# Kernel optimization log

Hardware: AMD Instinct MI355X
Metric: run time of the kernel (lower is better)

The kernel has to match this reference:

```python
import jax, jax.numpy as jnp
import numpy as np

N_ENTITIES = 100000
N_RELATIONS = 1000
D = 100   # embedding_size
K = 4     # tensor slices
B = 4096  # batch


def setup_inputs() -> dict:
    key = jax.random.key(0)
    k1, k2, k3, k4, k5, k6, k7, k8 = jax.random.split(key, 8)
    return {
        "heads": jax.random.randint(k1, (B,), 0, N_ENTITIES),
        "tails": jax.random.randint(k2, (B,), 0, N_ENTITIES),
        "relations": jax.random.randint(k3, (B,), 0, N_RELATIONS),
        # parameters, matching tf.random_uniform(0, 1)
        "entity_embedding": jax.random.uniform(k4, (N_ENTITIES, D), dtype=jnp.float32),
        "W": jax.random.uniform(k5, (N_RELATIONS, K, D, D), dtype=jnp.float32),
        "V": jax.random.uniform(k6, (N_RELATIONS, K, 2 * D), dtype=jnp.float32),
        "Bp": jax.random.uniform(k7, (N_RELATIONS, K), dtype=jnpp_f32 if False else jnp.float32),
        "U": jax.random.uniform(k8, (N_RELATIONS, K), dtype=jnp.float32),
    }


def reference(heads, tails, relations, entity_embedding, W, V, Bp, U):
    # gathers
    e1 = entity_embedding[heads]          # [B, D]
    e2 = entity_embedding[tails]          # [B, D]
    w = W[relations]                      # [B, K, D, D]
    v = V[relations]                      # [B, K, 2D]
    b = Bp[relations]                     # [B, K]
    u = U[relations]                      # [B, K]

    # g_a = v @ [e1; e2]
    e12 = jnp.concatenate([e1, e2], axis=1)           # [B, 2D]
    g_a = jnp.einsum('bkm,bm->bk', v, e12)            # [B, K]
    # g_b = e1^T W_k e2 (bilinear tensor product)
    g_b = jnp.einsum('bd,bkde,be->bk', e1, w, e2)     # [B, K]

    score = jnp.einsum('bk,bk->b', u, jnp.tanh(g_a + g_b + b))  # [B]
    pred = jax.nn.sigmoid(score)
    return pred
```

## Files before the change

kernel.cpp:

```cpp
#include <hip/hip_runtime.h>
#include <math.h>

#define D 100
#define K 4
#define NREL 1000
#define CH 8
#define NT 256

__global__ __launch_bounds__(1024) void group_kernel(const int* __restrict__ rels, int B,
                                                     int* __restrict__ start,
                                                     int* __restrict__ bucket) {
    __shared__ int cnt[NREL];
    __shared__ int sA[1024], sB[1024];
    const int tid = threadIdx.x;
    for (int i = tid; i < NREL; i += 1024) cnt[i] = 0;
    __syncthreads();
    for (int b = tid; b < B; b += 1024) atomicAdd(&cnt[rels[b]], 1);
    __syncthreads();
    const int v = (tid < NREL) ? cnt[tid] : 0;
    sA[tid] = v;
    __syncthreads();
    int* src = sA; int* dst = sB;
    for (int off = 1; off < 1024; off <<= 1) {
        int x = src[tid];
        if (tid >= off) x += src[tid - off];
        dst[tid] = x;
        __syncthreads();
        int* t = src; src = dst; dst = t;
    }
    const int excl = src[tid] - v;
    __syncthreads();
    if (tid < NREL) {
        start[tid] = excl;
        cnt[tid] = excl;
    }
    if (tid == 0) start[NREL] = B;
    __syncthreads();
    for (int b = tid; b < B; b += 1024) {
        int r = rels[b];
        int pos = atomicAdd(&cnt[r], 1);
        bucket[pos] = b;
    }
}

__global__ __launch_bounds__(NT) void ntn_main(
    const int* __restrict__ heads, const int* __restrict__ tails,
    const float* __restrict__ E, const float* __restrict__ W,
    const float* __restrict__ V, const float* __restrict__ Bp,
    const float* __restrict__ U, const int* __restrict__ start,
    const int* __restrict__ bucket, float* __restrict__ out)
{
    const int r = blockIdx.x;
    const int cs = start[r];
    const int n = start[r + 1] - cs;
    if (n <= 0) return;

    const int tid  = threadIdx.x;
    const int lane = tid & 63;
    const int k    = tid >> 6;
    const int dsub = lane / 25;
    const int c    = lane % 25;
    const bool active = (lane < 50);

    __shared__ float e12[CH][2 * D];
    __shared__ float red[K][CH];
    __shared__ int   bb[CH];

    const float* Wr = W + (size_t)r * K * D * D;
    const float* Vr = V + (size_t)r * K * 2 * D;

    for (int base = 0; base < n; base += CH) {
        const int m = min(CH, n - base);
        if (tid < CH) bb[tid] = (tid < m) ? bucket[cs + base + tid] : -1;
        __syncthreads();
        for (int idx = tid; idx < CH * 2 * D; idx += NT) {
            const int it = idx / (2 * D), j = idx % (2 * D);
            float val = 0.f;
            const int b = bb[it];
            if (b >= 0) {
                const int ent = (j < D) ? heads[b] : tails[b];
                val = E[(size_t)ent * D + (j < D ? j : j - D)];
            }
            e12[it][j] = val;
        }
        __syncthreads();

        float4 e2reg[CH];
        #pragma unroll
        for (int it = 0; it < CH; ++it)
            e2reg[it] = active ? *(const float4*)&e12[it][D + c * 4]
                               : make_float4(0.f, 0.f, 0.f, 0.f);

        float acc[CH];
        #pragma unroll
        for (int it = 0; it < CH; ++it) acc[it] = 0.f;

        const float* Wk = Wr + k * D * D;
        if (active) {
            #pragma unroll 2
            for (int dpair = 0; dpair < D / 2; ++dpair) {
                const int d = dpair * 2 + dsub;
                const float4 w = *(const float4*)&Wk[d * D + c * 4];
                const float e1d = e12[0][d];
                (void)e1d;
                #pragma unroll
                for (int it = 0; it < CH; ++it) {
                    float dot = w.x * e2reg[it].x + w.y * e2reg[it].y
                              + w.z * e2reg[it].z + w.w * e2reg[it].w;
                    acc[it] += dot * e12[it][d];
                }
            }
        }
        for (int j = lane; j < 2 * D; j += 64) {
            const float vv = Vr[k * 2 * D + j];
            #pragma unroll
            for (int it = 0; it < CH; ++it) acc[it] += vv * e12[it][j];
        }
        #pragma unroll
        for (int it = 0; it < CH; ++it) {
            float s = acc[it];
            #pragma unroll
            for (int off = 32; off > 0; off >>= 1) s += __shfl_down(s, off, 64);
            if (lane == 0) red[k][it] = s;
        }
        __syncthreads();
        if (tid < m) {
            float score = 0.f;
            #pragma unroll
            for (int kk = 0; kk < K; ++kk) {
                const float g = red[kk][tid] + Bp[r * K + kk];
                score += U[r * K + kk] * tanhf(g);
            }
            out[bb[tid]] = 1.f / (1.f + expf(-score));
        }
        __syncthreads();
    }
}

extern "C" void kernel_launch(void* const* d_in, const int* in_sizes, int n_in,
                              void* d_out, int out_size, void* d_ws, size_t ws_size,
                              hipStream_t stream) {
    const int*   heads = (const int*)d_in[0];
    const int*   tails = (const int*)d_in[1];
    const int*   rels  = (const int*)d_in[2];
    const float* E     = (const float*)d_in[3];
    const float* W     = (const float*)d_in[4];
    const float* V     = (const float*)d_in[5];
    const float* Bp    = (const float*)d_in[6];
    const float* U     = (const float*)d_in[7];
    float* out = (float*)d_out;

    const int B = in_sizes[0];
    int* start  = (int*)d_ws;
    int* bucket = start + 1024;

    group_kernel<<<1, 1024, 0, stream>>>(rels, B, start, bucket);
    ntn_main<<<NREL, NT, 0, stream>>>(heads, tails, E, W, V, Bp, U, start, bucket, out);
}
```

Baseline: 56.20 us.

## Fuse relation grouping into main kernel and split D across two wave halves

Drops the single-block counting-sort kernel. Each relation block now scans the relation array itself and collects matching batch indices into shared memory with an atomic counter. The block grows to 512 threads so two groups of four waves each cover half of the D rows of W, with partial sums combined at the end. This removes a serial launch and the workspace round trip, but every block rescans all B relations, and any relation with more than 64 matches silently drops the extra items.

Result: slower. 57.77 us (+2.8%).

```diff
diff --git a/kernel.cpp b/kernel.cpp
--- a/kernel.cpp
+++ b/kernel.cpp
@@ -5,79 +5,54 @@
 #define K 4
 #define NREL 1000
 #define CH 8
-#define NT 256
+#define NT 512
+#define MAXB 64
 
-__global__ __launch_bounds__(1024) void group_kernel(const int* __restrict__ rels, int B,
-                                                     int* __restrict__ start,
-                                                     int* __restrict__ bucket) {
-    __shared__ int cnt[NREL];
-    __shared__ int sA[1024], sB[1024];
-    const int tid = threadIdx.x;
-    for (int i = tid; i < NREL; i += 1024) cnt[i] = 0;
-    __syncthreads();
-    for (int b = tid; b < B; b += 1024) atomicAdd(&cnt[rels[b]], 1);
-    __syncthreads();
-    const int v = (tid < NREL) ? cnt[tid] : 0;
-    sA[tid] = v;
-    __syncthreads();
-    int* src = sA; int* dst = sB;
-    for (int off = 1; off < 1024; off <<= 1) {
-        int x = src[tid];
-        if (tid >= off) x += src[tid - off];
-        dst[tid] = x;
-        __syncthreads();
-        int* t = src; src = dst; dst = t;
-    }
-    const int excl = src[tid] - v;
-    __syncthreads();
-    if (tid < NREL) {
-        start[tid] = excl;
-        cnt[tid] = excl;
-    }
-    if (tid == 0) start[NREL] = B;
-    __syncthreads();
-    for (int b = tid; b < B; b += 1024) {
-        int r = rels[b];
-        int pos = atomicAdd(&cnt[r], 1);
-        bucket[pos] = b;
-    }
-}
-
-__global__ __launch_bounds__(NT) void ntn_main(
+__global__ __launch_bounds__(NT) void ntn_fused(
     const int* __restrict__ heads, const int* __restrict__ tails,
+    const int* __restrict__ rels,
     const float* __restrict__ E, const float* __restrict__ W,
     const float* __restrict__ V, const float* __restrict__ Bp,
-    const float* __restrict__ U, const int* __restrict__ start,
-    const int* __restrict__ bucket, float* __restrict__ out)
+    const float* __restrict__ U, float* __restrict__ out, int B)
 {
-    const int r = blockIdx.x;
-    const int cs = start[r];
-    const int n = start[r + 1] - cs;
-    if (n <= 0) return;
-
+    const int r    = blockIdx.x;
     const int tid  = threadIdx.x;
     const int lane = tid & 63;
-    const int k    = tid >> 6;
+    const int w    = tid >> 6;
+    const int k    = w & 3;
+    const int half = w >> 2;
     const int dsub = lane / 25;
     const int c    = lane % 25;
     const bool active = (lane < 50);
 
+    __shared__ int   bb[MAXB];
+    __shared__ int   cntS;
     __shared__ float e12[CH][2 * D];
-    __shared__ float red[K][CH];
-    __shared__ int   bb[CH];
+    __shared__ float red[8][CH];
 
-    const float* Wr = W + (size_t)r * K * D * D;
+    if (tid == 0) cntS = 0;
+    __syncthreads();
+    for (int b = tid; b < B; b += NT) {
+        if (rels[b] == r) {
+            int p = atomicAdd(&cntS, 1);
+            if (p < MAXB) bb[p] = b;
+        }
+    }
+    __syncthreads();
+    const int n = min(cntS, MAXB);
+    if (n == 0) return;
+
+    const float* Wk = W + ((size_t)r * K + k) * D * D;
     const float* Vr = V + (size_t)r * K * 2 * D;
 
     for (int base = 0; base < n; base += CH) {
         const int m = min(CH, n - base);
-        if (tid < CH) bb[tid] = (tid < m) ? bucket[cs + base + tid] : -1;
         __syncthreads();
         for (int idx = tid; idx < CH * 2 * D; idx += NT) {
             const int it = idx / (2 * D), j = idx % (2 * D);
             float val = 0.f;
-            const int b = bb[it];
-            if (b >= 0) {
+            if (it < m) {
+                const int b = bb[base + it];
                 const int ent = (j < D) ? heads[b] : tails[b];
                 val = E[(size_t)ent * D + (j < D ? j : j - D)];
             }
@@ -85,55 +60,52 @@
         }
         __syncthreads();
 
-        float4 e2reg[CH];
+        float4 e2r[CH];
         #pragma unroll
         for (int it = 0; it < CH; ++it)
-            e2reg[it] = active ? *(const float4*)&e12[it][D + c * 4]
-                               : make_float4(0.f, 0.f, 0.f, 0.f);
+            e2r[it] = active ? *(const float4*)&e12[it][D + c * 4]
+                             : make_float4(0.f, 0.f, 0.f, 0.f);
 
         float acc[CH];
         #pragma unroll
         for (int it = 0; it < CH; ++it) acc[it] = 0.f;
 
-        const float* Wk = Wr + k * D * D;
         if (active) {
-            #pragma unroll 2
-            for (int dpair = 0; dpair < D / 2; ++dpair) {
-                const int d = dpair * 2 + dsub;
-                const float4 w = *(const float4*)&Wk[d * D + c * 4];
-                const float e1d = e12[0][d];
-                (void)e1d;
+            #pragma unroll 5
+            for (int dp = 0; dp < 25; ++dp) {
+                const int d = half * 50 + dp * 2 + dsub;
+                const float4 wv = *(const float4*)&Wk[d * D + c * 4];
                 #pragma unroll
                 for (int it = 0; it < CH; ++it) {
-                    float dot = w.x * e2reg[it].x + w.y * e2reg[it].y
-                              + w.z * e2reg[it].z + w.w * e2reg[it].w;
-                    acc[it] += dot * e12[it][d];
+                    acc[it] += (wv.x * e2r[it].x + wv.y * e2r[it].y
+                              + wv.z * e2r[it].z + wv.w * e2r[it].w) * e12[it][d];
                 }
             }
         }
-        for (int j = lane; j < 2 * D; j += 64) {
-            const float vv = Vr[k * 2 * D + j];
-            #pragma unroll
-            for (int it = 0; it < CH; ++it) acc[it] += vv * e12[it][j];
+        if (half == 0) {
+            for (int j = lane; j < 2 * D; j += 64) {
+                const float vv = Vr[k * 2 * D + j];
+                #pragma unroll
+                for (int it = 0; it < CH; ++it) acc[it] += vv * e12[it][j];
+            }
         }
         #pragma unroll
         for (int it = 0; it < CH; ++it) {
             float s = acc[it];
             #pragma unroll
             for (int off = 32; off > 0; off >>= 1) s += __shfl_down(s, off, 64);
-            if (lane == 0) red[k][it] = s;
+            if (lane == 0) red[w][it] = s;
         }
         __syncthreads();
         if (tid < m) {
             float score = 0.f;
             #pragma unroll
             for (int kk = 0; kk < K; ++kk) {
-                const float g = red[kk][tid] + Bp[r * K + kk];
+                const float g = red[kk][tid] + red[4 + kk][tid] + Bp[r * K + kk];
                 score += U[r * K + kk] * tanhf(g);
             }
-            out[bb[tid]] = 1.f / (1.f + expf(-score));
+            out[bb[base + tid]] = 1.f / (1.f + expf(-score));
         }
-        __syncthreads();
     }
 }
 
@@ -151,9 +123,5 @@
     float* out = (float*)d_out;
 
     const int B = in_sizes[0];
-    int* start  = (int*)d_ws;
-    int* bucket = start + 1024;
-
-    group_kernel<<<1, 1024, 0, stream>>>(rels, B, start, bucket);
-    ntn_main<<<NREL, NT, 0, stream>>>(heads, tails, E, W, V, Bp, U, start, bucket, out);
+    ntn_fused<<<NREL, NT, 0, stream>>>(heads, tails, rels, E, W, V, Bp, U, out, B);
 }
```

## Split each relation's W across four blocks and parallelize grouping kernels

Applied to the files above, without the earlier changes.

Each relation's bilinear work is split across four blocks, each covering 25 rows of W. Each block writes partial sums to a workspace buffer, and a new epilogue kernel reduces them and applies tanh and the sigmoid. The single-block grouping kernel is replaced by multi-block zero, histogram, scan and scatter kernels, which spread the atomics over global memory. This raises parallelism from 1000 to 4000 blocks, at the cost of more kernel launches, extra global traffic for the partial sums, and the e12 gather being repeated in every split block.

Result: slower. 79.97 us (+42.3%).

```diff
diff --git a/kernel.cpp b/kernel.cpp
--- a/kernel.cpp
+++ b/kernel.cpp
@@ -7,17 +7,25 @@
 #define CH 8
 #define NT 256
 
-__global__ __launch_bounds__(1024) void group_kernel(const int* __restrict__ rels, int B,
-                                                     int* __restrict__ start,
-                                                     int* __restrict__ bucket) {
-    __shared__ int cnt[NREL];
+#define WS_CNT    0
+#define WS_START  1024
+#define WS_CURSOR 3072
+#define WS_BUCKET 4096
+#define WS_PART   8192
+
+__global__ void k_zero(int* ws) {
+    ws[WS_CNT + blockIdx.x * 256 + threadIdx.x] = 0;
+}
+
+__global__ void k_hist(const int* __restrict__ rels, int B, int* ws) {
+    int b = blockIdx.x * 256 + threadIdx.x;
+    if (b < B) atomicAdd(&ws[WS_CNT + rels[b]], 1);
+}
+
+__global__ __launch_bounds__(1024) void k_scan(int* ws, int B) {
     __shared__ int sA[1024], sB[1024];
     const int tid = threadIdx.x;
-    for (int i = tid; i < NREL; i += 1024) cnt[i] = 0;
-    __syncthreads();
-    for (int b = tid; b < B; b += 1024) atomicAdd(&cnt[rels[b]], 1);
-    __syncthreads();
-    const int v = (tid < NREL) ? cnt[tid] : 0;
+    const int v = (tid < NREL) ? ws[WS_CNT + tid] : 0;
     sA[tid] = v;
     __syncthreads();
     int* src = sA; int* dst = sB;
@@ -29,30 +37,31 @@
         int* t = src; src = dst; dst = t;
     }
     const int excl = src[tid] - v;
-    __syncthreads();
     if (tid < NREL) {
-        start[tid] = excl;
-        cnt[tid] = excl;
+        ws[WS_START + tid]  = excl;
+        ws[WS_CURSOR + tid] = excl;
     }
-    if (tid == 0) start[NREL] = B;
-    __syncthreads();
-    for (int b = tid; b < B; b += 1024) {
-        int r = rels[b];
-        int pos = atomicAdd(&cnt[r], 1);
-        bucket[pos] = b;
+    if (tid == 0) ws[WS_START + NREL] = B;
+}
+
+__global__ void k_scatter(const int* __restrict__ rels, int B, int* ws) {
+    int b = blockIdx.x * 256 + threadIdx.x;
+    if (b < B) {
+        int pos = atomicAdd(&ws[WS_CURSOR + rels[b]], 1);
+        ws[WS_BUCKET + pos] = b;
     }
 }
 
 __global__ __launch_bounds__(NT) void ntn_main(
     const int* __restrict__ heads, const int* __restrict__ tails,
     const float* __restrict__ E, const float* __restrict__ W,
-    const float* __restrict__ V, const float* __restrict__ Bp,
-    const float* __restrict__ U, const int* __restrict__ start,
-    const int* __restrict__ bucket, float* __restrict__ out)
+    const float* __restrict__ V, const int* __restrict__ ws,
+    float* __restrict__ part)
 {
-    const int r = blockIdx.x;
-    const int cs = start[r];
-    const int n = start[r + 1] - cs;
+    const int r = blockIdx.x >> 2;
+    const int g = blockIdx.x & 3;
+    const int cs = ws[WS_START + r];
+    const int n  = ws[WS_START + r + 1] - cs;
     if (n <= 0) return;
 
     const int tid  = threadIdx.x;
@@ -66,8 +75,9 @@
     __shared__ float red[K][CH];
     __shared__ int   bb[CH];
 
-    const float* Wr = W + (size_t)r * K * D * D;
-    const float* Vr = V + (size_t)r * K * 2 * D;
+    const float* Wk = W + ((size_t)r * K + k) * D * D + (size_t)g * 25 * D;
+    const float* Vk = V + ((size_t)r * K + k) * 2 * D;
+    const int* bucket = ws + WS_BUCKET;
 
     for (int base = 0; base < n; base += CH) {
         const int m = min(CH, n - base);
@@ -85,36 +95,35 @@
         }
         __syncthreads();
 
-        float4 e2reg[CH];
+        float4 e2r[CH];
         #pragma unroll
         for (int it = 0; it < CH; ++it)
-            e2reg[it] = active ? *(const float4*)&e12[it][D + c * 4]
-                               : make_float4(0.f, 0.f, 0.f, 0.f);
+            e2r[it] = active ? *(const float4*)&e12[it][D + c * 4]
+                             : make_float4(0.f, 0.f, 0.f, 0.f);
 
         float acc[CH];
         #pragma unroll
         for (int it = 0; it < CH; ++it) acc[it] = 0.f;
 
-        const float* Wk = Wr + k * D * D;
-        if (active) {
-            #pragma unroll 2
-            for (int dpair = 0; dpair < D / 2; ++dpair) {
-                const int d = dpair * 2 + dsub;
-                const float4 w = *(const float4*)&Wk[d * D + c * 4];
-                const float e1d = e12[0][d];
-                (void)e1d;
+        #pragma unroll
+        for (int dp = 0; dp < 13; ++dp) {
+            const int dd = dp * 2 + dsub;
+            if (active && dd < 25) {
+                const float4 wv = *(const float4*)&Wk[dd * D + c * 4];
                 #pragma unroll
                 for (int it = 0; it < CH; ++it) {
-                    float dot = w.x * e2reg[it].x + w.y * e2reg[it].y
-                              + w.z * e2reg[it].z + w.w * e2reg[it].w;
-                    acc[it] += dot * e12[it][d];
+                    acc[it] += (wv.x * e2r[it].x + wv.y * e2r[it].y
+                              + wv.z * e2r[it].z + wv.w * e2r[it].w)
+                             * e12[it][g * 25 + dd];
                 }
             }
         }
-        for (int j = lane; j < 2 * D; j += 64) {
-            const float vv = Vr[k * 2 * D + j];
-            #pragma unroll
-            for (int it = 0; it < CH; ++it) acc[it] += vv * e12[it][j];
+        if (g == 0) {
+            for (int j = lane; j < 2 * D; j += 64) {
+                const float vv = Vk[j];
+                #pragma unroll
+                for (int it = 0; it < CH; ++it) acc[it] += vv * e12[it][j];
+            }
         }
         #pragma unroll
         for (int it = 0; it < CH; ++it) {
@@ -124,17 +133,32 @@
             if (lane == 0) red[k][it] = s;
         }
         __syncthreads();
-        if (tid < m) {
-            float score = 0.f;
-            #pragma unroll
-            for (int kk = 0; kk < K; ++kk) {
-                const float g = red[kk][tid] + Bp[r * K + kk];
-                score += U[r * K + kk] * tanhf(g);
-            }
-            out[bb[tid]] = 1.f / (1.f + expf(-score));
+        if (tid < K * CH) {
+            const int kk = tid >> 3, it = tid & 7;
+            if (it < m)
+                part[(size_t)bb[it] * 16 + kk * 4 + g] = red[kk][it];
         }
         __syncthreads();
     }
+}
+
+__global__ __launch_bounds__(256) void ntn_epilogue(
+    const float* __restrict__ part, const int* __restrict__ rels,
+    const float* __restrict__ Bp, const float* __restrict__ U,
+    float* __restrict__ out, int B)
+{
+    const int b = blockIdx.x * 256 + threadIdx.x;
+    if (b >= B) return;
+    const int r = rels[b];
+    const float4* p4 = (const float4*)&part[(size_t)b * 16];
+    float score = 0.f;
+    #pragma unroll
+    for (int k = 0; k < K; ++k) {
+        const float4 p = p4[k];
+        const float gsum = (p.x + p.y) + (p.z + p.w) + Bp[r * K + k];
+        score += U[r * K + k] * tanhf(gsum);
+    }
+    out[b] = 1.f / (1.f + expf(-score));
 }
 
 extern "C" void kernel_launch(void* const* d_in, const int* in_sizes, int n_in,
@@ -151,9 +175,13 @@
     float* out = (float*)d_out;
 
     const int B = in_sizes[0];
-    int* start  = (int*)d_ws;
-    int* bucket = start + 1024;
+    int*   ws   = (int*)d_ws;
+    float* part = (float*)d_ws + WS_PART;
 
-    group_kernel<<<1, 1024, 0, stream>>>(rels, B, start, bucket);
-    ntn_main<<<NREL, NT, 0, stream>>>(heads, tails, E, W, V, Bp, U, start, bucket, out);
+    k_zero<<<4, 256, 0, stream>>>(ws);
+    k_hist<<<(B + 255) / 256, 256, 0, stream>>>(rels, B, ws);
+    k_scan<<<1, 1024, 0, stream>>>(ws, B);
+    k_scatter<<<(B + 255) / 256, 256, 0, stream>>>(rels, B, ws);
+    ntn_main<<<NREL * 4, NT, 0, stream>>>(heads, tails, E, W, V, ws, part);
+    ntn_epilogue<<<(B + 255) / 256, 256, 0, stream>>>(part, rels, Bp, U, out, B);
 }
```
